# Kernel optimization log

Measured on AMD Instinct MI355X. Metric: run time of the kernel, lower is better.

The kernel has to match this reference:

```python
import jax, jax.numpy as jnp
import numpy as np

N = 50000      # number of nodes
E = 800000     # number of edges (avg degree 16)
DIN = 128
DOUT = 128
EPS = 1e-06


def setup_inputs() -> dict:
    key = jax.random.key(0)
    ks = jax.random.split(key, 10)
    scale = 1.0 / np.sqrt(DIN)
    return {
        "mean": jax.random.normal(ks[0], (N, DIN), dtype=jnp.float32),
        "var": jax.random.uniform(ks[1], (N, DIN), dtype=jnp.float32),
        "W_mean": jax.random.normal(ks[2], (DIN, DOUT), dtype=jnp.float32) * scale,
        "b_mean": jax.random.normal(ks[3], (DOUT,), dtype=jnp.float32) * scale,
        "W_var": jax.random.normal(ks[4], (DIN, DOUT), dtype=jnp.float32) * scale,
        "b_var": jax.random.normal(ks[5], (DOUT,), dtype=jnp.float32) * scale,
        "adj0_w": jax.random.uniform(ks[6], (E,), dtype=jnp.float32),
        "adj1_w": jax.random.uniform(ks[7], (E,), dtype=jnp.float32),
        "edge_src": jax.random.randint(ks[8], (E,), 0, N, dtype=jnp.int32),
        "edge_dst": jax.random.randint(ks[9], (E,), 0, N, dtype=jnp.int32),
    }


def reference(mean, var, W_mean, b_mean, W_var, b_var, adj0_w, adj1_w, edge_src, edge_dst):
    # Dense projections (dropout is identity in eval mode)
    m = jax.nn.elu(mean @ W_mean + b_mean)            # [N, DOUT]
    v = jax.nn.relu(var @ W_var + b_var) + EPS        # [N, DOUT]
    # Elementwise attention gate
    att = jnp.exp(-v)
    m = m * att
    v = v * att * att
    # SpMM aggregation: out[dst] += w * x[src]  (COO edge list)
    n = mean.shape[0]
    out_m = jax.ops.segment_sum(adj0_w[:, None] * m[edge_src], edge_dst, num_segments=n)
    out_v = jax.ops.segment_sum(adj1_w[:, None] * v[edge_src], edge_dst, num_segments=n)
    return out_m, out_v
```

## Files before the change

kernel.cpp:

```cpp
#include <hip/hip_runtime.h>
#include <hip/hip_bf16.h>
#include <math.h>

#define N_NODES 50000
#define DIN     128
#define DOUT    128
#define EPS_    1e-6f
#define N_WAVES 3125
#define NBKT    196
#define EPB     4096
#define SLOT_CAP 5120

typedef __attribute__((ext_vector_type(8))) short  bf16x8;
typedef __attribute__((ext_vector_type(4))) float  f32x4;
typedef unsigned short ushort_t;

__device__ __forceinline__ ushort_t f2bf(float f) {
    unsigned u = __float_as_uint(f);
    return (ushort_t)((u + 0x7fffu + ((u >> 16) & 1u)) >> 16);
}

__global__ __launch_bounds__(256) void prep_w_kernel(
    const float* __restrict__ Wm, const float* __restrict__ Wv,
    ushort_t* __restrict__ fm, ushort_t* __restrict__ fv)
{
    const int gid = blockIdx.x * 256 + threadIdx.x;
    const int k = gid >> 7, n = gid & 127;
    const int ct = n >> 4, kk = k >> 5, quad = (k >> 3) & 3, j = k & 7;
    const int idx = ((ct * 4 + kk) * 64 + quad * 16 + (n & 15)) * 8 + j;
    fm[idx] = f2bf(Wm[gid]);
    fv[idx] = f2bf(Wv[gid]);
}

__global__ __launch_bounds__(256) void proj_mfma_kernel(
    const float* __restrict__ mean, const float* __restrict__ var,
    const float* __restrict__ bm,   const float* __restrict__ bv,
    const ushort_t* __restrict__ wfm, const ushort_t* __restrict__ wfv,
    ushort_t* __restrict__ mv)
{
    const int wave = blockIdx.x * 4 + (threadIdx.x >> 6);
    if (wave >= N_WAVES) return;
    const int lane = threadIdx.x & 63;
    const int row0 = wave * 16;
    const int kq   = lane >> 4;
    const int arow = row0 + (lane & 15);

    f32x4 accm[8], accv[8];
#pragma unroll
    for (int ct = 0; ct < 8; ++ct) {
        accm[ct] = (f32x4){0.f, 0.f, 0.f, 0.f};
        accv[ct] = (f32x4){0.f, 0.f, 0.f, 0.f};
    }

    const float* mrow = mean + (size_t)arow * DIN;
    const float* vrow = var  + (size_t)arow * DIN;

#pragma unroll
    for (int kk = 0; kk < 4; ++kk) {
        const int kb = kk * 32 + kq * 8;
        const float4 am0 = *(const float4*)(mrow + kb);
        const float4 am1 = *(const float4*)(mrow + kb + 4);
        const float4 av0 = *(const float4*)(vrow + kb);
        const float4 av1 = *(const float4*)(vrow + kb + 4);
        bf16x8 a_m, a_v;
        a_m[0]=f2bf(am0.x); a_m[1]=f2bf(am0.y); a_m[2]=f2bf(am0.z); a_m[3]=f2bf(am0.w);
        a_m[4]=f2bf(am1.x); a_m[5]=f2bf(am1.y); a_m[6]=f2bf(am1.z); a_m[7]=f2bf(am1.w);
        a_v[0]=f2bf(av0.x); a_v[1]=f2bf(av0.y); a_v[2]=f2bf(av0.z); a_v[3]=f2bf(av0.w);
        a_v[4]=f2bf(av1.x); a_v[5]=f2bf(av1.y); a_v[6]=f2bf(av1.z); a_v[7]=f2bf(av1.w);

#pragma unroll
        for (int ct = 0; ct < 8; ++ct) {
            const bf16x8 b_m = *(const bf16x8*)(wfm + ((size_t)(ct * 4 + kk) * 64 + lane) * 8);
            const bf16x8 b_v = *(const bf16x8*)(wfv + ((size_t)(ct * 4 + kk) * 64 + lane) * 8);
            accm[ct] = __builtin_amdgcn_mfma_f32_16x16x32_bf16(a_m, b_m, accm[ct], 0, 0, 0);
            accv[ct] = __builtin_amdgcn_mfma_f32_16x16x32_bf16(a_v, b_v, accv[ct], 0, 0, 0);
        }
    }

#pragma unroll
    for (int ct = 0; ct < 8; ++ct) {
        const int col = ct * 16 + (lane & 15);
        const float bmc = bm[col];
        const float bvc = bv[col];
        const int pbase = (col >> 1) * 4 + (col & 1);
#pragma unroll
        for (int r = 0; r < 4; ++r) {
            const int row = row0 + kq * 4 + r;
            float m = accm[ct][r] + bmc;
            m = (m > 0.0f) ? m : (expf(m) - 1.0f);
            float v = accv[ct][r] + bvc;
            v = ((v > 0.0f) ? v : 0.0f) + EPS_;
            const float att = expf(-v);
            ushort_t* rowp = mv + (size_t)row * 256;
            rowp[pbase]     = f2bf(m * att);
            rowp[pbase + 2] = f2bf(v * att * att);
        }
    }
}

__global__ __launch_bounds__(256) void bucketA_kernel(
    const int* __restrict__ src, const int* __restrict__ dst,
    const float* __restrict__ w0, const float* __restrict__ w1,
    int* __restrict__ gcur, uint2* __restrict__ slots, int E)
{
    __shared__ uint2 s_rec[EPB];
    __shared__ int   s_gpos[EPB];
    __shared__ int   s_hist[256];
    __shared__ int   s_scn[256];
    __shared__ int   s_cur[256];
    __shared__ int   s_base[256];

    const int t  = threadIdx.x;
    const int e0 = blockIdx.x * EPB;
    const int n  = min(EPB, E - e0);

    s_hist[t] = 0;
    __syncthreads();

    int   myb[16];
    uint2 myr[16];
#pragma unroll
    for (int j = 0; j < 16; ++j) {
        const int e = e0 + t + j * 256;
        if (e < E) {
            const int d = dst[e];
            const int b = d >> 8;
            myb[j] = b;
            myr[j].x = (unsigned)src[e] | ((unsigned)(d & 255) << 16);
            myr[j].y = (unsigned)f2bf(w0[e]) | ((unsigned)f2bf(w1[e]) << 16);
            atomicAdd(&s_hist[b], 1);
        } else myb[j] = -1;
    }
    __syncthreads();

    if (t < NBKT) {
        const int c = s_hist[t];
        s_base[t] = t * SLOT_CAP + (c ? atomicAdd(&gcur[t], c) : 0);
    }
    const int x = s_hist[t];
    s_scn[t] = x;
    __syncthreads();
    for (int off = 1; off < 256; off <<= 1) {
        const int v = (t >= off) ? s_scn[t - off] : 0;
        __syncthreads();
        s_scn[t] += v;
        __syncthreads();
    }
    const int excl = s_scn[t] - x;
    __syncthreads();
    s_scn[t] = excl;
    s_cur[t] = 0;
    __syncthreads();

#pragma unroll
    for (int j = 0; j < 16; ++j) {
        if (myb[j] >= 0) {
            const int r = atomicAdd(&s_cur[myb[j]], 1);
            const int p = s_scn[myb[j]] + r;
            s_rec[p]  = myr[j];
            s_gpos[p] = s_base[myb[j]] + r;
        }
    }
    __syncthreads();

    for (int i = t; i < n; i += 256)
        slots[s_gpos[i]] = s_rec[i];
}

__global__ __launch_bounds__(256) void bucket_scan_kernel(
    const int* __restrict__ gcur, int* __restrict__ bbase)
{
    __shared__ int s[256];
    const int t = threadIdx.x;
    const int x = (t < NBKT) ? gcur[t] : 0;
    s[t] = x;
    __syncthreads();
    for (int off = 1; off < 256; off <<= 1) {
        const int v = (t >= off) ? s[t - off] : 0;
        __syncthreads();
        s[t] += v;
        __syncthreads();
    }
    if (t < NBKT) bbase[t] = s[t] - x;
}

__global__ __launch_bounds__(256) void bucketB_kernel(
    const int* __restrict__ gcur, const int* __restrict__ bbase,
    const uint2* __restrict__ slots, uint2* __restrict__ final_e,
    int* __restrict__ node_start)
{
    __shared__ int s_hist[256];
    __shared__ int s_scn[256];
    __shared__ int s_cur[256];

    const int b    = blockIdx.x;
    const int t    = threadIdx.x;
    const int cnt  = gcur[b];
    const int base = bbase[b];
    const uint2* slot = slots + (size_t)b * SLOT_CAP;

    s_hist[t] = 0;
    __syncthreads();

    uint2 myr[20];
    int   myf[20];
    int   k = 0;
    for (int i = t; i < cnt; i += 256) {
        const uint2 r = slot[i];
        const int f = (r.x >> 16) & 255;
        myr[k] = r; myf[k] = f; ++k;
        atomicAdd(&s_hist[f], 1);
    }
    __syncthreads();

    const int x = s_hist[t];
    s_scn[t] = x;
    __syncthreads();
    for (int off = 1; off < 256; off <<= 1) {
        const int v = (t >= off) ? s_scn[t - off] : 0;
        __syncthreads();
        s_scn[t] += v;
        __syncthreads();
    }
    const int excl = s_scn[t] - x;
    __syncthreads();
    s_scn[t] = excl;
    __syncthreads();

    const int gidx = b * 256 + t;
    if (gidx <= N_NODES) node_start[gidx] = base + excl;

    s_cur[t] = excl;
    __syncthreads();

#pragma unroll
    for (int j = 0; j < 20; ++j) {
        if (j < k) {
            const int p = atomicAdd(&s_cur[myf[j]], 1);
            final_e[base + p] = myr[j];
        }
    }
}

__global__ __launch_bounds__(256) void agg_kernel(
    const ushort_t* __restrict__ mv,
    const uint2* __restrict__ edges, const int* __restrict__ node_start,
    float* __restrict__ out_m, float* __restrict__ out_v)
{
    const int node = blockIdx.x * 4 + (threadIdx.x >> 6);
    const int lane = threadIdx.x & 63;
    if (node >= N_NODES) return;

    const int j0 = node_start[node];
    const int j1 = node_start[node + 1];

    float m0 = 0.f, m1 = 0.f, v0 = 0.f, v1 = 0.f;

    int j = j0;
    for (; j + 4 <= j1; j += 4) {
        const uint2 r0 = edges[j + 0];
        const uint2 r1 = edges[j + 1];
        const uint2 r2 = edges[j + 2];
        const uint2 r3 = edges[j + 3];
        const uint2 g0 = ((const uint2*)(mv + (size_t)(r0.x & 0xffffu) * 256))[lane];
        const uint2 g1 = ((const uint2*)(mv + (size_t)(r1.x & 0xffffu) * 256))[lane];
        const uint2 g2 = ((const uint2*)(mv + (size_t)(r2.x & 0xffffu) * 256))[lane];
        const uint2 g3 = ((const uint2*)(mv + (size_t)(r3.x & 0xffffu) * 256))[lane];

        float a0, a1;
        a0 = __uint_as_float(r0.y << 16); a1 = __uint_as_float(r0.y & 0xffff0000u);
        m0 = fmaf(a0, __uint_as_float(g0.x << 16),         m0);
        m1 = fmaf(a0, __uint_as_float(g0.x & 0xffff0000u), m1);
        v0 = fmaf(a1, __uint_as_float(g0.y << 16),         v0);
        v1 = fmaf(a1, __uint_as_float(g0.y & 0xffff0000u), v1);
        a0 = __uint_as_float(r1.y << 16); a1 = __uint_as_float(r1.y & 0xffff0000u);
        m0 = fmaf(a0, __uint_as_float(g1.x << 16),         m0);
        m1 = fmaf(a0, __uint_as_float(g1.x & 0xffff0000u), m1);
        v0 = fmaf(a1, __uint_as_float(g1.y << 16),         v0);
        v1 = fmaf(a1, __uint_as_float(g1.y & 0xffff0000u), v1);
        a0 = __uint_as_float(r2.y << 16); a1 = __uint_as_float(r2.y & 0xffff0000u);
        m0 = fmaf(a0, __uint_as_float(g2.x << 16),         m0);
        m1 = fmaf(a0, __uint_as_float(g2.x & 0xffff0000u), m1);
        v0 = fmaf(a1, __uint_as_float(g2.y << 16),         v0);
        v1 = fmaf(a1, __uint_as_float(g2.y & 0xffff0000u), v1);
        a0 = __uint_as_float(r3.y << 16); a1 = __uint_as_float(r3.y & 0xffff0000u);
        m0 = fmaf(a0, __uint_as_float(g3.x << 16),         m0);
        m1 = fmaf(a0, __uint_as_float(g3.x & 0xffff0000u), m1);
        v0 = fmaf(a1, __uint_as_float(g3.y << 16),         v0);
        v1 = fmaf(a1, __uint_as_float(g3.y & 0xffff0000u), v1);
    }
    for (; j < j1; ++j) {
        const uint2 r = edges[j];
        const uint2 g = ((const uint2*)(mv + (size_t)(r.x & 0xffffu) * 256))[lane];
        const float a0 = __uint_as_float(r.y << 16);
        const float a1 = __uint_as_float(r.y & 0xffff0000u);
        m0 = fmaf(a0, __uint_as_float(g.x << 16),         m0);
        m1 = fmaf(a0, __uint_as_float(g.x & 0xffff0000u), m1);
        v0 = fmaf(a1, __uint_as_float(g.y << 16),         v0);
        v1 = fmaf(a1, __uint_as_float(g.y & 0xffff0000u), v1);
    }

    *(float2*)(out_m + (size_t)node * DOUT + lane * 2) = make_float2(m0, m1);
    *(float2*)(out_v + (size_t)node * DOUT + lane * 2) = make_float2(v0, v1);
}

extern "C" void kernel_launch(void* const* d_in, const int* in_sizes, int n_in,
                              void* d_out, int out_size, void* d_ws, size_t ws_size,
                              hipStream_t stream) {
    const float* mean = (const float*)d_in[0];
    const float* var  = (const float*)d_in[1];
    const float* Wm   = (const float*)d_in[2];
    const float* bm   = (const float*)d_in[3];
    const float* Wv   = (const float*)d_in[4];
    const float* bv   = (const float*)d_in[5];
    const float* a0   = (const float*)d_in[6];
    const float* a1   = (const float*)d_in[7];
    const int*   es   = (const int*)d_in[8];
    const int*   ed   = (const int*)d_in[9];
    const int    E    = in_sizes[6];

    char* ws = (char*)d_ws;
    ushort_t* mv        = (ushort_t*)ws;
    uint2* slots        = (uint2*)(ws + 25600000);
    uint2* final_e      = (uint2*)(ws + 33628160);
    int*   node_start   = (int*)  (ws + 40028160);
    int*   gcur         = (int*)  (ws + 40228164);
    int*   bbase        = (int*)  (ws + 40228948);
    ushort_t* wfm       = (ushort_t*)(ws + 40229744);
    ushort_t* wfv       = wfm + 16384;

    float* out_m = (float*)d_out;
    float* out_v = out_m + (size_t)N_NODES * DOUT;

    hipMemsetAsync(gcur, 0, NBKT * sizeof(int), stream);

    prep_w_kernel<<<64, 256, 0, stream>>>(Wm, Wv, wfm, wfv);

    proj_mfma_kernel<<<(N_WAVES + 3) / 4, 256, 0, stream>>>(
        mean, var, bm, bv, wfm, wfv, mv);

    bucketA_kernel<<<(E + EPB - 1) / EPB, 256, 0, stream>>>(
        es, ed, a0, a1, gcur, slots, E);
    bucket_scan_kernel<<<1, 256, 0, stream>>>(gcur, bbase);
    bucketB_kernel<<<NBKT, 256, 0, stream>>>(
        gcur, bbase, slots, final_e, node_start);

    agg_kernel<<<(N_NODES + 3) / 4, 256, 0, stream>>>(
        mv, final_e, node_start, out_m, out_v);
}
```

Measured before the change: 241.8 us.

## Fold memset and bucket scan into other kernels; split wave over edge pairs in aggregation

The gcur memset moves into prep_w_kernel, and the separate single-block bucket scan kernel is removed. Each bucketB block now computes its own base by reducing the counts of the preceding buckets. This cuts two launches from the pipeline. The aggregation kernel has each half-wave handle alternate edges with 16-byte gathers (8 bf16 per lane), then combines the halves with cross-half shuffles. This raises per-lane load width and edge-level parallelism, at the cost of idle half-waves on odd edge counts and extra shuffle/reduction work.

```diff
diff --git a/kernel.cpp b/kernel.cpp
--- a/kernel.cpp
+++ b/kernel.cpp
@@ -19,12 +19,16 @@
     unsigned u = __float_as_uint(f);
     return (ushort_t)((u + 0x7fffu + ((u >> 16) & 1u)) >> 16);
 }
+__device__ __forceinline__ float bflo(unsigned u) { return __uint_as_float(u << 16); }
+__device__ __forceinline__ float bfhi(unsigned u) { return __uint_as_float(u & 0xffff0000u); }
 
 __global__ __launch_bounds__(256) void prep_w_kernel(
     const float* __restrict__ Wm, const float* __restrict__ Wv,
-    ushort_t* __restrict__ fm, ushort_t* __restrict__ fv)
+    ushort_t* __restrict__ fm, ushort_t* __restrict__ fv,
+    int* __restrict__ gcur)
 {
     const int gid = blockIdx.x * 256 + threadIdx.x;
+    if (gid < NBKT) gcur[gid] = 0;
     const int k = gid >> 7, n = gid & 127;
     const int ct = n >> 4, kk = k >> 5, quad = (k >> 3) & 3, j = k & 7;
     const int idx = ((ct * 4 + kk) * 64 + quad * 16 + (n & 15)) * 8 + j;
@@ -167,40 +171,29 @@
         slots[s_gpos[i]] = s_rec[i];
 }
 
-__global__ __launch_bounds__(256) void bucket_scan_kernel(
-    const int* __restrict__ gcur, int* __restrict__ bbase)
-{
-    __shared__ int s[256];
-    const int t = threadIdx.x;
-    const int x = (t < NBKT) ? gcur[t] : 0;
-    s[t] = x;
-    __syncthreads();
-    for (int off = 1; off < 256; off <<= 1) {
-        const int v = (t >= off) ? s[t - off] : 0;
-        __syncthreads();
-        s[t] += v;
-        __syncthreads();
-    }
-    if (t < NBKT) bbase[t] = s[t] - x;
-}
-
 __global__ __launch_bounds__(256) void bucketB_kernel(
-    const int* __restrict__ gcur, const int* __restrict__ bbase,
+    const int* __restrict__ gcur,
     const uint2* __restrict__ slots, uint2* __restrict__ final_e,
     int* __restrict__ node_start)
 {
     __shared__ int s_hist[256];
     __shared__ int s_scn[256];
     __shared__ int s_cur[256];
-
-    const int b    = blockIdx.x;
-    const int t    = threadIdx.x;
+    __shared__ int s_red[256];
+
+    const int b = blockIdx.x;
+    const int t = threadIdx.x;
+
+    s_red[t] = (t < b) ? gcur[t] : 0;
+    s_hist[t] = 0;
+    __syncthreads();
+    for (int off = 128; off > 0; off >>= 1) {
+        if (t < off) s_red[t] += s_red[t + off];
+        __syncthreads();
+    }
+    const int base = s_red[0];
     const int cnt  = gcur[b];
-    const int base = bbase[b];
     const uint2* slot = slots + (size_t)b * SLOT_CAP;
-
-    s_hist[t] = 0;
-    __syncthreads();
 
     uint2 myr[20];
     int   myf[20];
@@ -224,8 +217,6 @@
     }
     const int excl = s_scn[t] - x;
     __syncthreads();
-    s_scn[t] = excl;
-    __syncthreads();
 
     const int gidx = b * 256 + t;
     if (gidx <= N_NODES) node_start[gidx] = base + excl;
@@ -242,6 +233,14 @@
     }
 }
 
+#define PAIR_FMA(RW, G) do {                                                 \
+    const float a0 = bflo(RW), a1 = bfhi(RW);                                \
+    am0 = fmaf(a0, bflo((G).x), am0); am1 = fmaf(a0, bfhi((G).x), am1);      \
+    av0 = fmaf(a1, bflo((G).y), av0); av1 = fmaf(a1, bfhi((G).y), av1);      \
+    am2 = fmaf(a0, bflo((G).z), am2); am3 = fmaf(a0, bfhi((G).z), am3);      \
+    av2 = fmaf(a1, bflo((G).w), av2); av3 = fmaf(a1, bfhi((G).w), av3);      \
+} while (0)
+
 __global__ __launch_bounds__(256) void agg_kernel(
     const ushort_t* __restrict__ mv,
     const uint2* __restrict__ edges, const int* __restrict__ node_start,
@@ -249,59 +248,68 @@
 {
     const int node = blockIdx.x * 4 + (threadIdx.x >> 6);
     const int lane = threadIdx.x & 63;
+    const int half = lane >> 5;
+    const int l    = lane & 31;
     if (node >= N_NODES) return;
 
     const int j0 = node_start[node];
     const int j1 = node_start[node + 1];
 
-    float m0 = 0.f, m1 = 0.f, v0 = 0.f, v1 = 0.f;
+    float am0=0.f, am1=0.f, am2=0.f, am3=0.f;
+    float av0=0.f, av1=0.f, av2=0.f, av3=0.f;
 
     int j = j0;
-    for (; j + 4 <= j1; j += 4) {
-        const uint2 r0 = edges[j + 0];
-        const uint2 r1 = edges[j + 1];
-        const uint2 r2 = edges[j + 2];
-        const uint2 r3 = edges[j + 3];
-        const uint2 g0 = ((const uint2*)(mv + (size_t)(r0.x & 0xffffu) * 256))[lane];
-        const uint2 g1 = ((const uint2*)(mv + (size_t)(r1.x & 0xffffu) * 256))[lane];
-        const uint2 g2 = ((const uint2*)(mv + (size_t)(r2.x & 0xffffu) * 256))[lane];
-        const uint2 g3 = ((const uint2*)(mv + (size_t)(r3.x & 0xffffu) * 256))[lane];
-
-        float a0, a1;
-        a0 = __uint_as_float(r0.y << 16); a1 = __uint_as_float(r0.y & 0xffff0000u);
-        m0 = fmaf(a0, __uint_as_float(g0.x << 16),         m0);
-        m1 = fmaf(a0, __uint_as_float(g0.x & 0xffff0000u), m1);
-        v0 = fmaf(a1, __uint_as_float(g0.y << 16),         v0);
-        v1 = fmaf(a1, __uint_as_float(g0.y & 0xffff0000u), v1);
-        a0 = __uint_as_float(r1.y << 16); a1 = __uint_as_float(r1.y & 0xffff0000u);
-        m0 = fmaf(a0, __uint_as_float(g1.x << 16),         m0);
-        m1 = fmaf(a0, __uint_as_float(g1.x & 0xffff0000u), m1);
-        v0 = fmaf(a1, __uint_as_float(g1.y << 16),         v0);
-        v1 = fmaf(a1, __uint_as_float(g1.y & 0xffff0000u), v1);
-        a0 = __uint_as_float(r2.y << 16); a1 = __uint_as_float(r2.y & 0xffff0000u);
-        m0 = fmaf(a0, __uint_as_float(g2.x << 16),         m0);
-        m1 = fmaf(a0, __uint_as_float(g2.x & 0xffff0000u), m1);
-        v0 = fmaf(a1, __uint_as_float(g2.y << 16),         v0);
-        v1 = fmaf(a1, __uint_as_float(g2.y & 0xffff0000u), v1);
-        a0 = __uint_as_float(r3.y << 16); a1 = __uint_as_float(r3.y & 0xffff0000u);
-        m0 = fmaf(a0, __uint_as_float(g3.x << 16),         m0);
-        m1 = fmaf(a0, __uint_as_float(g3.x & 0xffff0000u), m1);
-        v0 = fmaf(a1, __uint_as_float(g3.y << 16),         v0);
-        v1 = fmaf(a1, __uint_as_float(g3.y & 0xffff0000u), v1);
-    }
-    for (; j < j1; ++j) {
+
+    if ((j & 1) && j < j1) {
         const uint2 r = edges[j];
-        const uint2 g = ((const uint2*)(mv + (size_t)(r.x & 0xffffu) * 256))[lane];
-        const float a0 = __uint_as_float(r.y << 16);
-        const float a1 = __uint_as_float(r.y & 0xffff0000u);
-        m0 = fmaf(a0, __uint_as_float(g.x << 16),         m0);
-        m1 = fmaf(a0, __uint_as_float(g.x & 0xffff0000u), m1);
-        v0 = fmaf(a1, __uint_as_float(g.y << 16),         v0);
-        v1 = fmaf(a1, __uint_as_float(g.y & 0xffff0000u), v1);
-    }
-
-    *(float2*)(out_m + (size_t)node * DOUT + lane * 2) = make_float2(m0, m1);
-    *(float2*)(out_v + (size_t)node * DOUT + lane * 2) = make_float2(v0, v1);
+        const unsigned rw = half ? 0u : r.y;
+        const uint4 g = *(const uint4*)(mv + (size_t)(r.x & 0xffffu) * 256 + l * 8);
+        PAIR_FMA(rw, g);
+        ++j;
+    }
+
+    for (; j + 8 <= j1; j += 8) {
+        const uint4 e0 = *(const uint4*)(edges + j + 0);
+        const uint4 e1 = *(const uint4*)(edges + j + 2);
+        const uint4 e2 = *(const uint4*)(edges + j + 4);
+        const uint4 e3 = *(const uint4*)(edges + j + 6);
+        const unsigned s0 = half ? e0.z : e0.x, w0 = half ? e0.w : e0.y;
+        const unsigned s1 = half ? e1.z : e1.x, w1 = half ? e1.w : e1.y;
+        const unsigned s2 = half ? e2.z : e2.x, w2 = half ? e2.w : e2.y;
+        const unsigned s3 = half ? e3.z : e3.x, w3 = half ? e3.w : e3.y;
+        const uint4 g0 = *(const uint4*)(mv + (size_t)(s0 & 0xffffu) * 256 + l * 8);
+        const uint4 g1 = *(const uint4*)(mv + (size_t)(s1 & 0xffffu) * 256 + l * 8);
+        const uint4 g2 = *(const uint4*)(mv + (size_t)(s2 & 0xffffu) * 256 + l * 8);
+        const uint4 g3 = *(const uint4*)(mv + (size_t)(s3 & 0xffffu) * 256 + l * 8);
+        PAIR_FMA(w0, g0);
+        PAIR_FMA(w1, g1);
+        PAIR_FMA(w2, g2);
+        PAIR_FMA(w3, g3);
+    }
+
+    for (; j + 2 <= j1; j += 2) {
+        const uint4 e = *(const uint4*)(edges + j);
+        const unsigned s = half ? e.z : e.x, w = half ? e.w : e.y;
+        const uint4 g = *(const uint4*)(mv + (size_t)(s & 0xffffu) * 256 + l * 8);
+        PAIR_FMA(w, g);
+    }
+
+    if (j < j1) {
+        const uint2 r = edges[j];
+        const unsigned rw = half ? 0u : r.y;
+        const uint4 g = *(const uint4*)(mv + (size_t)(r.x & 0xffffu) * 256 + l * 8);
+        PAIR_FMA(rw, g);
+    }
+
+    am0 += __shfl_xor(am0, 32); am1 += __shfl_xor(am1, 32);
+    am2 += __shfl_xor(am2, 32); am3 += __shfl_xor(am3, 32);
+    av0 += __shfl_xor(av0, 32); av1 += __shfl_xor(av1, 32);
+    av2 += __shfl_xor(av2, 32); av3 += __shfl_xor(av3, 32);
+
+    if (half == 0) {
+        *(float4*)(out_m + (size_t)node * DOUT + l * 4) = make_float4(am0, am1, am2, am3);
+        *(float4*)(out_v + (size_t)node * DOUT + l * 4) = make_float4(av0, av1, av2, av3);
+    }
 }
 
 extern "C" void kernel_launch(void* const* d_in, const int* in_sizes, int n_in,
@@ -324,26 +332,22 @@
     uint2* slots        = (uint2*)(ws + 25600000);
     uint2* final_e      = (uint2*)(ws + 33628160);
     int*   node_start   = (int*)  (ws + 40028160);
-    int*   gcur         = (int*)  (ws + 40228164);
-    int*   bbase        = (int*)  (ws + 40228948);
-    ushort_t* wfm       = (ushort_t*)(ws + 40229744);
+    int*   gcur         = (int*)  (ws + 40228176);
+    ushort_t* wfm       = (ushort_t*)(ws + 40228976);
     ushort_t* wfv       = wfm + 16384;
 
     float* out_m = (float*)d_out;
     float* out_v = out_m + (size_t)N_NODES * DOUT;
 
-    hipMemsetAsync(gcur, 0, NBKT * sizeof(int), stream);
-
-    prep_w_kernel<<<64, 256, 0, stream>>>(Wm, Wv, wfm, wfv);
+    prep_w_kernel<<<64, 256, 0, stream>>>(Wm, Wv, wfm, wfv, gcur);
 
     proj_mfma_kernel<<<(N_WAVES + 3) / 4, 256, 0, stream>>>(
         mean, var, bm, bv, wfm, wfv, mv);
 
     bucketA_kernel<<<(E + EPB - 1) / EPB, 256, 0, stream>>>(
         es, ed, a0, a1, gcur, slots, E);
-    bucket_scan_kernel<<<1, 256, 0, stream>>>(gcur, bbase);
     bucketB_kernel<<<NBKT, 256, 0, stream>>>(
-        gcur, bbase, slots, final_e, node_start);
+        gcur, slots, final_e, node_start);
 
     agg_kernel<<<(N_NODES + 3) / 4, 256, 0, stream>>>(
         mv, final_e, node_start, out_m, out_v);
```

Result: faster. 232.7 us (-3.8%).
